# Kernel tuning notes

Measured on AMD Instinct MI355X. Metric: run time of the kernel, lower is better.

## Reference

```python
import jax, jax.numpy as jnp
import numpy as np

SIZE = 128
BATCH = 64
STEEPNESS = 10.0


def _odd_even_indices(n):
    """Odd-even transposition sorting network: n layers of disjoint adjacent pairs.
    All layers are padded to k = n//2 pairs with self-pairs (i,i)=(0,0), which are
    exact no-ops under the soft compare-exchange (matches pass-through wires of the
    original network)."""
    k = n // 2
    ia, ib = [], []
    for layer in range(n):
        start = layer % 2
        pa = list(range(start, n - 1, 2))
        pb = [i + 1 for i in pa]
        while len(pa) < k:  # pad with no-op self-pairs
            pa.append(0)
            pb.append(0)
        ia.append(pa)
        ib.append(pb)
    return jnp.asarray(np.array(ia, np.int32)), jnp.asarray(np.array(ib, np.int32))


def setup_inputs() -> dict:
    key = jax.random.key(0)
    return {"vectors": jax.random.normal(key, (BATCH, SIZE), dtype=jnp.float32)}


def _soft_sort(vectors):
    Bsz, n = vectors.shape
    ia, ib = _odd_even_indices(n)  # [n_layers, k] each
    x0 = vectors
    # X[b, i, j] = soft probability mass of input element i at output slot j,
    # i.e. the invariant  x[b] == vectors[b] @ X[b]  holds after every layer.
    X0 = jnp.tile(jnp.eye(n, dtype=vectors.dtype)[None], (Bsz, 1, 1))
    inv_pi = jnp.float32(1.0 / np.pi)

    def step(carry, idx):
        x, X = carry
        a_idx, b_idx = idx
        a = x[:, a_idx]  # [B, k]
        b = x[:, b_idx]  # [B, k]
        # Cauchy CDF relaxation of the comparison (module default distribution)
        alpha = jnp.arctan(STEEPNESS * (b - a)) * inv_pi + 0.5
        x = x.at[:, a_idx].set(alpha * a + (1.0 - alpha) * b)        # soft min
        x = x.at[:, b_idx].set((1.0 - alpha) * a + alpha * b)        # soft max
        A = X[:, :, a_idx]   # [B, n, k] columns feeding the 'a' wires
        Bc = X[:, :, b_idx]  # [B, n, k] columns feeding the 'b' wires
        w = alpha[:, None, :]
        X = X.at[:, :, a_idx].set(w * A + (1.0 - w) * Bc)
        X = X.at[:, :, b_idx].set((1.0 - w) * A + w * Bc)
        return (x, X), None

    (x, X), _ = jax.lax.scan(step, (x0, X0), (ia, ib))
    return x, X


def reference(vectors):
    # Returns (softly sorted values [B, n], relaxed permutation matrix [B, n, n])
    return _soft_sort(vectors)
```

## Files before the change

### kernel.cpp

```cpp
#include <hip/hip_runtime.h>
#include <math.h>

#define SIZE 128
#define BATCH 64
#define STEEP 10.0f
#define G 8
#define NG 8

typedef float v2f __attribute__((ext_vector_type(2)));

__device__ __forceinline__ v2f v2bc(float s) { return (v2f){s, s}; }
__device__ __forceinline__ v2f v2fma(v2f a, v2f b, v2f c) {
    return __builtin_elementwise_fma(a, b, c);
}

template<int CTRL>
__device__ __forceinline__ float dpp_mov(float x) {
    return __int_as_float(__builtin_amdgcn_update_dpp(
        __float_as_int(x), __float_as_int(x), CTRL, 0xf, 0xf, false));
}

__device__ __forceinline__ float alpha_from_delta(float delta) {
    const float C0 =  0.31830265f;
    const float C1 = -0.10587730f;
    const float C2 =  0.06160680f;
    const float C3 = -0.03706173f;
    const float C4 =  0.01676007f;
    const float C5 = -0.00373098f;
    float t  = STEEP * delta;
    float at = fabsf(t);
    bool inv = at > 1.0f;
    float z  = inv ? __builtin_amdgcn_rcpf(at) : at;
    float z2 = z * z, z4 = z2 * z2;
    float p0 = fmaf(C1, z2, C0);
    float p1 = fmaf(C3, z2, C2);
    float p2 = fmaf(C5, z2, C4);
    float q  = fmaf(fmaf(p2, z4, p1), z4, p0) * z;
    float r  = inv ? 0.5f - q : q;
    return 0.5f + copysignf(r, t);
}

__global__ __launch_bounds__(192) void soft_sort_fused(
    const float* __restrict__ vec, float* __restrict__ out)
{
    __shared__ float alds[2][2 * G * 64];

    const int tid    = threadIdx.x;
    const int lane   = tid & 63;
    const int wave   = tid >> 6;
    const int batch  = blockIdx.x >> 3;
    const int rowgrp = blockIdx.x & 7;

    if (wave == 2) {
        __builtin_amdgcn_s_setprio(1);
        const int c0 = 2 * lane;
        const float2 xv = *reinterpret_cast<const float2*>(vec + batch * SIZE + c0);
        float xa = xv.x, xb = xv.y;
        const bool hasR = (lane < 63);
        const bool hasL = (lane > 0);

        for (int grp = 0; grp < NG; ++grp) {
            float* buf = &alds[grp & 1][0];
#pragma unroll
            for (int j = 0; j < G; ++j) {
                const float d  = xb - xa;
                const float ae = alpha_from_delta(d);
                buf[(2 * j) * 64 + lane] = ae;
                const float nxa0 = fmaf(-ae, d, xb);
                const float nxb0 = fmaf( ae, d, xa);
                const float xnext = dpp_mov<0x130>(nxa0);
                float ao = alpha_from_delta(xnext - nxb0);
                ao = hasR ? ao : 1.0f;
                buf[(2 * j + 1) * 64 + lane] = ao;
                float aoL = dpp_mov<0x138>(ao);
                aoL = hasL ? aoL : 1.0f;
                const float xprev = dpp_mov<0x138>(nxb0);
                xb = fmaf(ao,  nxb0 - xnext, xnext);
                xa = fmaf(aoL, nxa0 - xprev, xprev);
            }
            __syncthreads();
        }
        if (rowgrp == 0)
            *reinterpret_cast<float2*>(out + batch * SIZE + c0) = make_float2(xa, xb);
    } else {
        const int chunk = lane & 15;
        const int rsub  = lane >> 4;
        const int row0  = rowgrp * 16 + wave * 8 + rsub * 2;
        const int c8    = chunk * 8;
        const int q4    = chunk * 4;
        const int qm    = (chunk > 0) ? q4 - 1 : 63;

        v2f v[8];
#pragma unroll
        for (int j = 0; j < 8; ++j)
            v[j] = (v2f){ (row0     == c8 + j) ? 1.0f : 0.0f,
                          (row0 + 1 == c8 + j) ? 1.0f : 0.0f };

        for (int grp = 0; grp < NG; ++grp) {
            __syncthreads();
            const float* buf = &alds[grp & 1][0];
            float4 ae = *reinterpret_cast<const float4*>(buf + q4);
            float4 ao = *reinterpret_cast<const float4*>(buf + 64 + q4);
            float  aL = buf[64 + qm];
#pragma unroll
            for (int j = 0; j < G; ++j) {
                const int nj = (j < G - 1) ? j + 1 : j;
                const float4 ae_n = *reinterpret_cast<const float4*>(buf + (2 * nj) * 64 + q4);
                const float4 ao_n = *reinterpret_cast<const float4*>(buf + (2 * nj + 1) * 64 + q4);
                const float  aL_n = buf[(2 * nj + 1) * 64 + qm];

                v2f A, B, d;
#define CXP(i0, i1, al)                                                        \
                A = v[i0]; B = v[i1]; d = A - B;                               \
                v[i0] = v2fma(v2bc(al), d, B);                                 \
                v[i1] = v2fma(v2bc(-(al)), d, A);
                CXP(0, 1, ae.x)
                CXP(2, 3, ae.y)
                CXP(4, 5, ae.z)
                CXP(6, 7, ae.w)
                v2f nb0, pb7;
                nb0.x = dpp_mov<0x101>(v[0].x);
                nb0.y = dpp_mov<0x101>(v[0].y);
                pb7.x = dpp_mov<0x111>(v[7].x);
                pb7.y = dpp_mov<0x111>(v[7].y);
                CXP(1, 2, ao.x)
                CXP(3, 4, ao.y)
                CXP(5, 6, ao.z)
#undef CXP
                v[7] = v2fma(v2bc(ao.w), v[7] - nb0, nb0);
                v[0] = v2fma(v2bc(aL),   v[0] - pb7, pb7);

                ae = ae_n; ao = ao_n; aL = aL_n;
            }
        }

        float* __restrict__ X0 = out + BATCH * SIZE + ((size_t)batch * SIZE + row0) * SIZE + c8;
        float* __restrict__ X1 = X0 + SIZE;
        *reinterpret_cast<float4*>(X0)     = make_float4(v[0].x, v[1].x, v[2].x, v[3].x);
        *reinterpret_cast<float4*>(X0 + 4) = make_float4(v[4].x, v[5].x, v[6].x, v[7].x);
        *reinterpret_cast<float4*>(X1)     = make_float4(v[0].y, v[1].y, v[2].y, v[3].y);
        *reinterpret_cast<float4*>(X1 + 4) = make_float4(v[4].y, v[5].y, v[6].y, v[7].y);
    }
}

extern "C" void kernel_launch(void* const* d_in, const int* in_sizes, int n_in,
                              void* d_out, int out_size, void* d_ws, size_t ws_size,
                              hipStream_t stream) {
    const float* vec = (const float*)d_in[0];
    float* out = (float*)d_out;
    (void)in_sizes; (void)n_in; (void)d_ws; (void)ws_size; (void)out_size;

    hipLaunchKernelGGL(soft_sort_fused, dim3(BATCH * 8), dim3(192), 0, stream,
                       vec, out);
}
```

Before: 65.04 us.

## Recompute alphas redundantly per wave and lay out X by columns

Removes the producer wave, the LDS alpha buffer and the per-group barriers. Every wave now recomputes the value recurrence itself and applies the alphas directly to four rows of X, using a column-per-lane layout that matches the x-lane layout. The neighbour exchange for odd layers uses DPP row shifts. This trades redundant transcendental-like alpha work in every wave for no synchronisation and no LDS traffic.

```diff
diff --git a/kernel.cpp b/kernel.cpp
--- a/kernel.cpp
+++ b/kernel.cpp
@@ -4,8 +4,7 @@
 #define SIZE 128
 #define BATCH 64
 #define STEEP 10.0f
-#define G 8
-#define NG 8
+#define NLP 64
 
 typedef float v2f __attribute__((ext_vector_type(2)));
 
@@ -40,106 +39,75 @@
     return 0.5f + copysignf(r, t);
 }
 
-__global__ __launch_bounds__(192) void soft_sort_fused(
+__global__ __launch_bounds__(256) void soft_sort_cols(
     const float* __restrict__ vec, float* __restrict__ out)
 {
-    __shared__ float alds[2][2 * G * 64];
+    const int tid   = threadIdx.x;
+    const int lane  = tid & 63;
+    const int wave  = tid >> 6;
+    const int batch = blockIdx.x >> 3;
+    const int oct   = blockIdx.x & 7;
+    const int rg    = oct * 4 + wave;
+    const int row0  = rg * 4;
 
-    const int tid    = threadIdx.x;
-    const int lane   = tid & 63;
-    const int wave   = tid >> 6;
-    const int batch  = blockIdx.x >> 3;
-    const int rowgrp = blockIdx.x & 7;
+    const int c0i = 2 * lane;
+    const float2 xv = *reinterpret_cast<const float2*>(vec + batch * SIZE + c0i);
+    float xa = xv.x, xb = xv.y;
+    const bool hasR = (lane < 63);
+    const bool hasL = (lane > 0);
 
-    if (wave == 2) {
-        __builtin_amdgcn_s_setprio(1);
-        const int c0 = 2 * lane;
-        const float2 xv = *reinterpret_cast<const float2*>(vec + batch * SIZE + c0);
-        float xa = xv.x, xb = xv.y;
-        const bool hasR = (lane < 63);
-        const bool hasL = (lane > 0);
+    v2f cA[2], cB[2];
+#pragma unroll
+    for (int p = 0; p < 2; ++p) {
+        cA[p] = (v2f){ (row0 + 2 * p     == c0i) ? 1.0f : 0.0f,
+                       (row0 + 2 * p + 1 == c0i) ? 1.0f : 0.0f };
+        cB[p] = (v2f){ (row0 + 2 * p     == c0i + 1) ? 1.0f : 0.0f,
+                       (row0 + 2 * p + 1 == c0i + 1) ? 1.0f : 0.0f };
+    }
 
-        for (int grp = 0; grp < NG; ++grp) {
-            float* buf = &alds[grp & 1][0];
+#pragma unroll 4
+    for (int j = 0; j < NLP; ++j) {
+        const float d  = xb - xa;
+        const float ae = alpha_from_delta(d);
+        const float nxa0 = fmaf(-ae, d, xb);
+        const float nxb0 = fmaf( ae, d, xa);
 #pragma unroll
-            for (int j = 0; j < G; ++j) {
-                const float d  = xb - xa;
-                const float ae = alpha_from_delta(d);
-                buf[(2 * j) * 64 + lane] = ae;
-                const float nxa0 = fmaf(-ae, d, xb);
-                const float nxb0 = fmaf( ae, d, xa);
-                const float xnext = dpp_mov<0x130>(nxa0);
-                float ao = alpha_from_delta(xnext - nxb0);
-                ao = hasR ? ao : 1.0f;
-                buf[(2 * j + 1) * 64 + lane] = ao;
-                float aoL = dpp_mov<0x138>(ao);
-                aoL = hasL ? aoL : 1.0f;
-                const float xprev = dpp_mov<0x138>(nxb0);
-                xb = fmaf(ao,  nxb0 - xnext, xnext);
-                xa = fmaf(aoL, nxa0 - xprev, xprev);
-            }
-            __syncthreads();
+        for (int p = 0; p < 2; ++p) {
+            const v2f A = cA[p], B = cB[p], dd = A - B;
+            cA[p] = v2fma(v2bc(ae),  dd, B);
+            cB[p] = v2fma(v2bc(-ae), dd, A);
         }
-        if (rowgrp == 0)
-            *reinterpret_cast<float2*>(out + batch * SIZE + c0) = make_float2(xa, xb);
-    } else {
-        const int chunk = lane & 15;
-        const int rsub  = lane >> 4;
-        const int row0  = rowgrp * 16 + wave * 8 + rsub * 2;
-        const int c8    = chunk * 8;
-        const int q4    = chunk * 4;
-        const int qm    = (chunk > 0) ? q4 - 1 : 63;
+        const float xnext = dpp_mov<0x130>(nxa0);
+        float ao = alpha_from_delta(xnext - nxb0);
+        ao = hasR ? ao : 1.0f;
+        float aoL = dpp_mov<0x138>(ao);
+        aoL = hasL ? aoL : 1.0f;
+        const float xprev = dpp_mov<0x138>(nxb0);
+        xb = fmaf(ao,  nxb0 - xnext, xnext);
+        xa = fmaf(aoL, nxa0 - xprev, xprev);
+#pragma unroll
+        for (int p = 0; p < 2; ++p) {
+            v2f nb, pb;
+            nb.x = dpp_mov<0x130>(cA[p].x);
+            nb.y = dpp_mov<0x130>(cA[p].y);
+            pb.x = dpp_mov<0x138>(cB[p].x);
+            pb.y = dpp_mov<0x138>(cB[p].y);
+            cB[p] = v2fma(v2bc(ao),  cB[p] - nb, nb);
+            cA[p] = v2fma(v2bc(aoL), cA[p] - pb, pb);
+        }
+    }
 
-        v2f v[8];
+    if (oct == 0 && wave == 0)
+        *reinterpret_cast<float2*>(out + batch * SIZE + c0i) = make_float2(xa, xb);
+
+    float* __restrict__ Xb = out + BATCH * SIZE + (size_t)batch * SIZE * SIZE;
 #pragma unroll
-        for (int j = 0; j < 8; ++j)
-            v[j] = (v2f){ (row0     == c8 + j) ? 1.0f : 0.0f,
-                          (row0 + 1 == c8 + j) ? 1.0f : 0.0f };
-
-        for (int grp = 0; grp < NG; ++grp) {
-            __syncthreads();
-            const float* buf = &alds[grp & 1][0];
-            float4 ae = *reinterpret_cast<const float4*>(buf + q4);
-            float4 ao = *reinterpret_cast<const float4*>(buf + 64 + q4);
-            float  aL = buf[64 + qm];
-#pragma unroll
-            for (int j = 0; j < G; ++j) {
-                const int nj = (j < G - 1) ? j + 1 : j;
-                const float4 ae_n = *reinterpret_cast<const float4*>(buf + (2 * nj) * 64 + q4);
-                const float4 ao_n = *reinterpret_cast<const float4*>(buf + (2 * nj + 1) * 64 + q4);
-                const float  aL_n = buf[(2 * nj + 1) * 64 + qm];
-
-                v2f A, B, d;
-#define CXP(i0, i1, al)                                                        \
-                A = v[i0]; B = v[i1]; d = A - B;                               \
-                v[i0] = v2fma(v2bc(al), d, B);                                 \
-                v[i1] = v2fma(v2bc(-(al)), d, A);
-                CXP(0, 1, ae.x)
-                CXP(2, 3, ae.y)
-                CXP(4, 5, ae.z)
-                CXP(6, 7, ae.w)
-                v2f nb0, pb7;
-                nb0.x = dpp_mov<0x101>(v[0].x);
-                nb0.y = dpp_mov<0x101>(v[0].y);
-                pb7.x = dpp_mov<0x111>(v[7].x);
-                pb7.y = dpp_mov<0x111>(v[7].y);
-                CXP(1, 2, ao.x)
-                CXP(3, 4, ao.y)
-                CXP(5, 6, ao.z)
-#undef CXP
-                v[7] = v2fma(v2bc(ao.w), v[7] - nb0, nb0);
-                v[0] = v2fma(v2bc(aL),   v[0] - pb7, pb7);
-
-                ae = ae_n; ao = ao_n; aL = aL_n;
-            }
-        }
-
-        float* __restrict__ X0 = out + BATCH * SIZE + ((size_t)batch * SIZE + row0) * SIZE + c8;
-        float* __restrict__ X1 = X0 + SIZE;
-        *reinterpret_cast<float4*>(X0)     = make_float4(v[0].x, v[1].x, v[2].x, v[3].x);
-        *reinterpret_cast<float4*>(X0 + 4) = make_float4(v[4].x, v[5].x, v[6].x, v[7].x);
-        *reinterpret_cast<float4*>(X1)     = make_float4(v[0].y, v[1].y, v[2].y, v[3].y);
-        *reinterpret_cast<float4*>(X1 + 4) = make_float4(v[4].y, v[5].y, v[6].y, v[7].y);
+    for (int p = 0; p < 2; ++p) {
+        const int r0 = row0 + 2 * p;
+        *reinterpret_cast<float2*>(Xb + (size_t)r0 * SIZE + c0i) =
+            make_float2(cA[p].x, cB[p].x);
+        *reinterpret_cast<float2*>(Xb + (size_t)(r0 + 1) * SIZE + c0i) =
+            make_float2(cA[p].y, cB[p].y);
     }
 }
 
@@ -150,6 +118,6 @@
     float* out = (float*)d_out;
     (void)in_sizes; (void)n_in; (void)d_ws; (void)ws_size; (void)out_size;
 
-    hipLaunchKernelGGL(soft_sort_fused, dim3(BATCH * 8), dim3(192), 0, stream,
+    hipLaunchKernelGGL(soft_sort_cols, dim3(BATCH * 8), dim3(256), 0, stream,
                        vec, out);
 }
```

Measured after the change: 71.21 us. 1.09x slower.
